# Kernel optimization log

Measured on AMD Instinct MI355X. Metric: run time of the kernel, lower is better.

The kernel has to match this reference:

```python
import jax, jax.numpy as jnp
import numpy as np

U, I, E, B, NNZ, N_LAYERS = 100000, 50000, 64, 3, 2400000, 3
N = U + I


def setup_inputs() -> dict:
    key = jax.random.key(0)
    ks = jax.random.split(key, 7)
    return {
        "user_emb": jax.random.normal(ks[0], (U, E), jnp.float32) * 0.1,
        "item_emb": jax.random.normal(ks[1], (I, E), jnp.float32) * 0.1,
        "W1": jax.random.normal(ks[2], (B, E, E // 4), jnp.float32) * 0.25,
        "W2": jax.random.normal(ks[3], (B, E // 4, 1), jnp.float32) * 0.5,
        "adj_vals": jax.random.uniform(ks[4], (B, NNZ), jnp.float32) * (1.0 / 16.0),
        "adj_rows": jax.random.randint(ks[5], (B, NNZ), 0, N, jnp.int32),
        "adj_cols": jax.random.randint(ks[6], (B, NNZ), 0, N, jnp.int32),
    }


def _spmm(vals, rows, cols, x):
    # sparse [N,N] @ dense [N,E] via gather + segment-sum over destination rows
    return jax.ops.segment_sum(vals[:, None] * x[cols], rows, num_segments=N)


def _propagate(vals, rows, cols, ego):
    acc = ego
    cur = ego
    for _ in range(N_LAYERS):
        cur = _spmm(vals, rows, cols, cur)
        acc = acc + cur
    return acc / float(N_LAYERS + 1)  # mean over stacked layer embeddings


def reference(user_emb, item_emb, W1, W2, adj_vals, adj_rows, adj_cols):
    ego = jnp.concatenate([user_emb, item_emb], axis=0)  # [N, E]
    # per-behavior LightGCN propagation (loop over small fixed B)
    beh = jnp.stack(
        [_propagate(adj_vals[i], adj_rows[i], adj_cols[i], ego) for i in range(B)],
        axis=1,
    )  # [N, B, E]

    def att_one(w1, w2):
        score = jnp.squeeze(jnp.tanh(beh @ w1) @ w2, -1)  # [N, B]
        a = jax.nn.softmax(score, axis=1)
        return jnp.einsum("nb,nbe->ne", a, beh)  # [N, E]

    bias = jax.vmap(att_one)(W1, W2)  # [B, N, E]
    user_beh_emb = bias[:, :U]  # [B, U, E]
    item_beh_emb = bias[:, U:]  # [B, I, E]
    return user_beh_emb, item_beh_emb
```

## Files before the change

kernel.cpp:

```cpp
#include <hip/hip_runtime.h>

#define UCNT 100000
#define ICNT 50000
#define BB   3
#define NNZE 2400000
#define NN   150000

#define P1B   16
#define PR1   9375
#define CAP1  156000
#define NBKT  (BB * P1B)
#define DEPTH 192
#define FCH   64
#define P1BLK 375
#define P1CH  6400
#define CSTR  16
#define HJ    8
#define P2J   128

#define SCAN_CHUNK 4096
#define CPB ((NN + SCAN_CHUNK - 1) / SCAN_CHUNK)

__global__ __launch_bounds__(256) void k_zero2(int* __restrict__ cnt,
                                               int* __restrict__ gcnt){
  long long i = (long long)blockIdx.x * blockDim.x + threadIdx.x;
  if (i < (long long)BB * NN) cnt[i] = 0;
  long long j = i - (long long)BB * NN;
  if (j >= 0 && j < NBKT * CSTR) gcnt[j] = 0;
}

__global__ __launch_bounds__(256) void k_cvt(const float* __restrict__ ue,
                                             const float* __restrict__ ie,
                                             unsigned* __restrict__ egob){
  long long w = (long long)blockIdx.x * blockDim.x + threadIdx.x;
  if (w >= (long long)NN * 32) return;
  long long n = w >> 5;
  int pr = (int)(w & 31);
  const float* src = (n < UCNT) ? (ue + n * 64) : (ie + (n - UCNT) * 64);
  float2 v = *(const float2*)(src + pr * 2);
  unsigned a = __float_as_uint(v.x); a += 0x7FFF + ((a >> 16) & 1);
  unsigned b = __float_as_uint(v.y); b += 0x7FFF + ((b >> 16) & 1);
  egob[w] = (a >> 16) | (b & 0xFFFF0000u);
}

__global__ __launch_bounds__(256) void k_p1(const int* __restrict__ rows,
                                            const int* __restrict__ cols,
                                            const float* __restrict__ vals,
                                            int* __restrict__ gcnt,
                                            int2* __restrict__ stg){
  __shared__ int2 lbuf[P1B][DEPTH];
  __shared__ int  lcnt[P1B];
  int tid = threadIdx.x, lane = tid & 63, wv = tid >> 6;
  int beh = blockIdx.x / P1BLK;
  int blk = blockIdx.x - beh * P1BLK;
  long long ebase = (long long)beh * NNZE + (long long)blk * P1CH;
  if (tid < P1B) lcnt[tid] = 0;
  __syncthreads();

  for (int r = 0; r < 13; ++r){
    int off = r * 512 + tid * 2;
    if (off < P1CH){
      long long i = ebase + off;
      int2  rr = *(const int2*)(rows + i);
      int2  cc = *(const int2*)(cols + i);
      float2 vv = *(const float2*)(vals + i);
      #pragma unroll
      for (int k = 0; k < 2; ++k){
        int row = k ? rr.y : rr.x;
        int col = k ? cc.y : cc.x;
        float val = k ? vv.y : vv.x;
        int part = row / PR1;
        int2 ent = make_int2(((row - part * PR1) << 18) | col,
                             __float_as_int(val));
        int p = atomicAdd(&lcnt[part], 1);
        if (p < DEPTH){
          lbuf[part][p] = ent;
        } else {
          int gb = atomicAdd(&gcnt[(beh * P1B + part) * CSTR], 1);
          if (gb < CAP1)
            stg[(long long)(beh * P1B + part) * CAP1 + gb] = ent;
        }
      }
    }
    __syncthreads();
    for (int pp = wv; pp < P1B; pp += 4){
      int n = min(lcnt[pp], DEPTH);
      int nf = n & ~(FCH - 1);
      if (nf > 0){
        int gb = 0;
        if (lane == 0) gb = atomicAdd(&gcnt[(beh * P1B + pp) * CSTR], nf);
        gb = __shfl(gb, 0);
        long long sb = (long long)(beh * P1B + pp) * CAP1;
        for (int k = lane; k < nf; k += 64)
          if (gb + k < CAP1) stg[sb + gb + k] = lbuf[pp][k];
        int res = n - nf;
        int2 t;
        if (lane < res) t = lbuf[pp][nf + lane];
        if (lane < res) lbuf[pp][lane] = t;
        if (lane == 0) lcnt[pp] = res;
      }
    }
    __syncthreads();
  }
  for (int pp = wv; pp < P1B; pp += 4){
    int n = min(lcnt[pp], DEPTH);
    if (n > 0){
      int gb = 0;
      if (lane == 0) gb = atomicAdd(&gcnt[(beh * P1B + pp) * CSTR], n);
      gb = __shfl(gb, 0);
      long long sb = (long long)(beh * P1B + pp) * CAP1;
      if (lane < n && gb + lane < CAP1) stg[sb + gb + lane] = lbuf[pp][lane];
    }
  }
}

__global__ __launch_bounds__(256) void k_hist3(const int* __restrict__ gcnt,
                                               const int2* __restrict__ stg,
                                               int* __restrict__ cnt){
  __shared__ int h[PR1];
  int bucket = blockIdx.x / HJ;
  int j = blockIdx.x - bucket * HJ;
  for (int i = threadIdx.x; i < PR1; i += 256) h[i] = 0;
  __syncthreads();
  int n = min(gcnt[bucket * CSTR], CAP1);
  const int2* st = stg + (long long)bucket * CAP1;
  int chunk = (n + HJ - 1) / HJ;
  int lo = j * chunk, hi = min(n, lo + chunk);
  for (int i = lo + threadIdx.x; i < hi; i += 256)
    atomicAdd(&h[(unsigned)st[i].x >> 18], 1);
  __syncthreads();
  int beh = bucket / P1B, part = bucket - beh * P1B;
  int* c = cnt + (long long)beh * NN + part * PR1;
  for (int i = threadIdx.x; i < PR1; i += 256){
    int v = h[i];
    if (v) atomicAdd(&c[i], v);
  }
}

__global__ __launch_bounds__(1024) void k_bsum(const int* __restrict__ cnt,
                                               int* __restrict__ bsum){
  int blk = blockIdx.x;
  int b = blk / CPB, ch = blk - b * CPB;
  const int* src = cnt + (long long)b * NN;
  int base = ch * SCAN_CHUNK + threadIdx.x * 4;
  int s = 0;
  #pragma unroll
  for (int k = 0; k < 4; ++k){
    int i = base + k;
    if (i < NN) s += src[i];
  }
  __shared__ int sd[1024];
  sd[threadIdx.x] = s;
  __syncthreads();
  for (int off = 512; off > 0; off >>= 1){
    if (threadIdx.x < off) sd[threadIdx.x] += sd[threadIdx.x + off];
    __syncthreads();
  }
  if (threadIdx.x == 0) bsum[blk] = sd[0];
}

__global__ __launch_bounds__(64) void k_bscan(const int* __restrict__ bsum,
                                              int* __restrict__ boff,
                                              int* __restrict__ rp){
  int b = threadIdx.x;
  if (b >= BB) return;
  int run = 0;
  for (int c = 0; c < CPB; ++c){
    boff[b * CPB + c] = run;
    run += bsum[b * CPB + c];
  }
  rp[(long long)b * (NN + 1) + NN] = run;
}

__global__ __launch_bounds__(1024) void k_scan2(const int* __restrict__ cnt,
                                                const int* __restrict__ boff,
                                                int* __restrict__ rp,
                                                int* __restrict__ tp){
  int blk = blockIdx.x;
  int b = blk / CPB, ch = blk - b * CPB;
  const int* src = cnt + (long long)b * NN;
  int* rpo = rp + (long long)b * (NN + 1);
  int* tpo = tp + (long long)b * NN;
  int base = ch * SCAN_CHUNK + threadIdx.x * 4;
  int v[4]; int tsum = 0;
  #pragma unroll
  for (int k = 0; k < 4; ++k){
    int i = base + k;
    v[k] = (i < NN) ? src[i] : 0;
    tsum += v[k];
  }
  __shared__ int sd[1024];
  sd[threadIdx.x] = tsum;
  __syncthreads();
  for (int off = 1; off < 1024; off <<= 1){
    int t = (threadIdx.x >= off) ? sd[threadIdx.x - off] : 0;
    __syncthreads();
    sd[threadIdx.x] += t;
    __syncthreads();
  }
  int excl = boff[blk] + sd[threadIdx.x] - tsum;
  #pragma unroll
  for (int k = 0; k < 4; ++k){
    int i = base + k;
    if (i < NN){ rpo[i] = excl; tpo[i] = excl; }
    excl += v[k];
  }
}

__global__ __launch_bounds__(256) void k_p2(const int* __restrict__ gcnt,
                                            const int2* __restrict__ stg,
                                            int* __restrict__ tp,
                                            int2* __restrict__ cpk,
                                            int L){
  int x = blockIdx.x & 7;
  int j = blockIdx.x >> 3;
  int bucket = L * 8 + x;
  int n = min(gcnt[bucket * CSTR], CAP1);
  int beh = bucket / P1B, part = bucket - beh * P1B;
  int rowbase = part * PR1;
  const int2* st = stg + (long long)bucket * CAP1;
  int* tpb = tp + (long long)beh * NN;
  int2* dst = cpk + (long long)beh * NNZE;
  int chunk = (n + P2J - 1) / P2J;
  int lo = j * chunk, hi = min(n, lo + chunk);
  for (int i = lo + threadIdx.x; i < hi; i += 256){
    int2 e = st[i];
    int row = rowbase + (int)((unsigned)e.x >> 18);
    int col = e.x & 0x3FFFF;
    int pos = atomicAdd(&tpb[row], 1);
    dst[pos] = make_int2(col, e.y);
  }
}

#define GB(NK)                                                              \
  {                                                                         \
    int   c[NK]; float v[NK]; float x[NK];                                  \
    _Pragma("unroll")                                                       \
    for (int k = 0; k < NK; ++k){                                           \
      int2 q = pk[e + k];                                                   \
      c[k] = __builtin_amdgcn_readfirstlane(q.x);                           \
      v[k] = __int_as_float(__builtin_amdgcn_readfirstlane(q.y));           \
    }                                                                       \
    _Pragma("unroll")                                                       \
    for (int k = 0; k < NK; ++k){                                           \
      unsigned w = xb[(long long)c[k] * 32 + (lane >> 1)];                  \
      x[k] = __uint_as_float((lane & 1) ? (w & 0xFFFF0000u) : (w << 16));   \
    }                                                                       \
    _Pragma("unroll")                                                       \
    for (int k = 0; k < NK; ++k){                                           \
      if (k & 1) sB = fmaf(v[k], x[k], sB);                                 \
      else       sA = fmaf(v[k], x[k], sA);                                 \
    }                                                                       \
    e += NK;                                                                \
  }

template<int MODE>
__global__ __launch_bounds__(256) void k_spmmB(const int* __restrict__ rp,
                                               const int2* __restrict__ cpk,
                                               const unsigned* __restrict__ xb,
                                               const float* __restrict__ ue,
                                               const float* __restrict__ ie,
                                               unsigned* __restrict__ dstb,
                                               float* __restrict__ acc,
                                               int b){
  int row = blockIdx.x * (blockDim.x >> 6) + (threadIdx.x >> 6);
  int lane = threadIdx.x & 63;
  row = __builtin_amdgcn_readfirstlane(row);
  const int* rpo = rp + (long long)b * (NN + 1);
  int s0 = __builtin_amdgcn_readfirstlane(rpo[row]);
  int s1 = __builtin_amdgcn_readfirstlane(rpo[row + 1]);
  const int2* pk = cpk + (long long)b * NNZE;
  float sA = 0.f, sB = 0.f;
  int e = s0;
  while (e + 16 <= s1) GB(16)
  if (e + 8 <= s1) GB(8)
  if (e + 4 <= s1) GB(4)
  if (e + 2 <= s1) GB(2)
  if (e < s1){
    int2 q = pk[e];
    int   c0 = __builtin_amdgcn_readfirstlane(q.x);
    float v0 = __int_as_float(__builtin_amdgcn_readfirstlane(q.y));
    unsigned w = xb[(long long)c0 * 32 + (lane >> 1)];
    float x0 = __uint_as_float((lane & 1) ? (w & 0xFFFF0000u) : (w << 16));
    sA = fmaf(v0, x0, sA);
  }
  float s = sA + sB;
  long long o = ((long long)b * NN + row) * 64 + lane;
  if (MODE == 0){
    float ego = (row < UCNT) ? ue[(long long)row * 64 + lane]
                             : ie[(long long)(row - UCNT) * 64 + lane];
    acc[o] = ego + s;
  } else {
    acc[o] += s;
  }
  if (MODE != 2){
    unsigned u = __float_as_uint(s);
    u += 0x7FFF + ((u >> 16) & 1);
    unsigned hb = u >> 16;
    unsigned ot = (unsigned)__shfl_xor((int)hb, 1);
    if (!(lane & 1))
      dstb[(long long)row * 32 + (lane >> 1)] = hb | (ot << 16);
  }
}

__device__ __forceinline__ float fast_tanh(float x){
  float xc = fminf(fmaxf(x, -15.f), 15.f);
  float t = __expf(2.f * xc);
  return (t - 1.f) / (t + 1.f);
}

__global__ __launch_bounds__(256) void k_score(const float* __restrict__ acc,
                                               const float* __restrict__ W1,
                                               const float* __restrict__ W2,
                                               float* __restrict__ scbuf){
  __shared__ float sW1[BB * 64 * 16];
  __shared__ float sW2[BB * 16];
  for (int i = threadIdx.x; i < BB * 64 * 16; i += blockDim.x) sW1[i] = W1[i];
  if (threadIdx.x < BB * 16) sW2[threadIdx.x] = W2[threadIdx.x];
  __syncthreads();
  int t = blockIdx.x * blockDim.x + threadIdx.x;
  if (t >= BB * NN) return;
  int b = t / NN;
  int n = t - b * NN;

  const float4* src = (const float4*)(acc + ((long long)b * NN + n) * 64);
  float4 v[16];
  #pragma unroll
  for (int c = 0; c < 16; ++c){
    v[c] = src[c];
    v[c].x *= 0.25f; v[c].y *= 0.25f; v[c].z *= 0.25f; v[c].w *= 0.25f;
  }
  for (int h = 0; h < BB; ++h){
    float hid[16];
    #pragma unroll
    for (int k = 0; k < 16; ++k) hid[k] = 0.f;
    #pragma unroll
    for (int c = 0; c < 16; ++c){
      const float* w = &sW1[h * 1024 + c * 64];
      #pragma unroll
      for (int k = 0; k < 16; ++k){
        hid[k] += v[c].x * w[k] + v[c].y * w[16 + k]
                + v[c].z * w[32 + k] + v[c].w * w[48 + k];
      }
    }
    float s = 0.f;
    #pragma unroll
    for (int k = 0; k < 16; ++k) s += fast_tanh(hid[k]) * sW2[h * 16 + k];
    scbuf[(long long)n * 9 + h * 3 + b] = s;
  }
}

__global__ __launch_bounds__(256) void k_att2(const float* __restrict__ acc,
                                              const float* __restrict__ scbuf,
                                              float* __restrict__ out){
  int t = blockIdx.x * blockDim.x + threadIdx.x;
  int n = t >> 4;
  int c = t & 15;
  if (n >= NN) return;
  float sc[9];
  #pragma unroll
  for (int i = 0; i < 9; ++i) sc[i] = scbuf[(long long)n * 9 + i];

  float a[BB][BB];
  #pragma unroll
  for (int h = 0; h < BB; ++h){
    float s0 = sc[h * 3], s1 = sc[h * 3 + 1], s2 = sc[h * 3 + 2];
    float m = fmaxf(fmaxf(s0, s1), s2);
    float e0 = __expf(s0 - m), e1 = __expf(s1 - m), e2 = __expf(s2 - m);
    float inv = 1.f / (e0 + e1 + e2);
    a[h][0] = e0 * inv; a[h][1] = e1 * inv; a[h][2] = e2 * inv;
  }
  float4 x0 = ((const float4*)(acc + ((long long)0 * NN + n) * 64))[c];
  float4 x1 = ((const float4*)(acc + ((long long)1 * NN + n) * 64))[c];
  float4 x2 = ((const float4*)(acc + ((long long)2 * NN + n) * 64))[c];
  x0.x *= 0.25f; x0.y *= 0.25f; x0.z *= 0.25f; x0.w *= 0.25f;
  x1.x *= 0.25f; x1.y *= 0.25f; x1.z *= 0.25f; x1.w *= 0.25f;
  x2.x *= 0.25f; x2.y *= 0.25f; x2.z *= 0.25f; x2.w *= 0.25f;
  #pragma unroll
  for (int h = 0; h < BB; ++h){
    float4 o;
    o.x = a[h][0]*x0.x + a[h][1]*x1.x + a[h][2]*x2.x;
    o.y = a[h][0]*x0.y + a[h][1]*x1.y + a[h][2]*x2.y;
    o.z = a[h][0]*x0.z + a[h][1]*x1.z + a[h][2]*x2.z;
    o.w = a[h][0]*x0.w + a[h][1]*x1.w + a[h][2]*x2.w;
    long long dst;
    if (n < UCNT) dst = ((long long)h * UCNT + n) * 64;
    else          dst = (long long)BB * UCNT * 64 + ((long long)h * ICNT + (n - UCNT)) * 64;
    ((float4*)(out + dst))[c] = o;
  }
}

extern "C" void kernel_launch(void* const* d_in, const int* in_sizes, int n_in,
                              void* d_out, int out_size, void* d_ws, size_t ws_size,
                              hipStream_t stream){
  const float* ue   = (const float*)d_in[0];
  const float* ie   = (const float*)d_in[1];
  const float* W1   = (const float*)d_in[2];
  const float* W2   = (const float*)d_in[3];
  const float* vals = (const float*)d_in[4];
  const int*   rows = (const int*)d_in[5];
  const int*   cols = (const int*)d_in[6];
  float* out = (float*)d_out;

  char* ws = (char*)d_ws;
  size_t off = 0;
  auto alloc = [&](size_t bytes){ void* p = ws + off; off += (bytes + 255) & ~(size_t)255; return p; };
  float*    acc   = (float*)alloc((size_t)BB * NN * 64 * 4);
  int2*     cpk   = (int2*)alloc((size_t)BB * NNZE * 8);
  int2*     stg   = (int2*)alloc((size_t)NBKT * CAP1 * 8);
  unsigned* egob  = (unsigned*)alloc((size_t)NN * 32 * 4);
  unsigned* layb0 = (unsigned*)alloc((size_t)NN * 32 * 4);
  unsigned* layb1 = (unsigned*)alloc((size_t)NN * 32 * 4);
  int*      rp    = (int*)alloc((size_t)BB * (NN + 1) * 4);
  int*      tp    = (int*)alloc((size_t)BB * NN * 4);
  int*      cnt   = (int*)alloc((size_t)BB * NN * 4);
  int*      bsum  = (int*)alloc((size_t)BB * CPB * 4);
  int*      boff  = (int*)alloc((size_t)BB * CPB * 4);
  int*      gcnt  = (int*)alloc((size_t)NBKT * CSTR * 4);
  float*    scbuf = (float*)alloc((size_t)NN * 9 * 4);
  (void)ws_size; (void)in_sizes; (void)n_in; (void)out_size;

  k_zero2<<<(BB * NN + NBKT * CSTR + 255) / 256, 256, 0, stream>>>(cnt, gcnt);
  k_cvt<<<(int)(((long long)NN * 32 + 255) / 256), 256, 0, stream>>>(ue, ie, egob);
  k_p1<<<BB * P1BLK, 256, 0, stream>>>(rows, cols, vals, gcnt, stg);
  k_hist3<<<NBKT * HJ, 256, 0, stream>>>(gcnt, stg, cnt);
  k_bsum<<<BB * CPB, 1024, 0, stream>>>(cnt, bsum);
  k_bscan<<<1, 64, 0, stream>>>(bsum, boff, rp);
  k_scan2<<<BB * CPB, 1024, 0, stream>>>(cnt, boff, rp, tp);
  for (int L = 0; L < 6; ++L)
    k_p2<<<8 * P2J, 256, 0, stream>>>(gcnt, stg, tp, cpk, L);

  for (int b = 0; b < BB; ++b){
    k_spmmB<0><<<NN / 4, 256, 0, stream>>>(rp, cpk, egob,  ue, ie, layb0, acc, b);
    k_spmmB<1><<<NN / 4, 256, 0, stream>>>(rp, cpk, layb0, ue, ie, layb1, acc, b);
    k_spmmB<2><<<NN / 4, 256, 0, stream>>>(rp, cpk, layb1, ue, ie, nullptr, acc, b);
  }
  k_score<<<(BB * NN + 255) / 256, 256, 0, stream>>>(acc, W1, W2, scbuf);
  k_att2<<<(NN * 16) / 256, 256, 0, stream>>>(acc, scbuf, out);
}
```

Measured before the change: 1.120 ms.

## Store per-layer bf16 outputs and drop fp32 accumulator read-modify-write in SpMM

The SpMM kernels no longer read the ego embedding or read-modify-write a large fp32 accumulator. Each layer now writes only its bf16 output into a 9-slot layer buffer. The score and attention kernels rebuild the layer mean by summing the bf16 ego and the three layer outputs. This cuts fp32 traffic in the propagation loop but adds more reads in the score and attention kernels. It also lowers accuracy, since the sum now uses the ego and the last layer in bf16 instead of fp32.

After: 1.054 ms. 1.06x faster.

```diff
diff --git a/kernel.cpp b/kernel.cpp
--- a/kernel.cpp
+++ b/kernel.cpp
@@ -20,6 +20,9 @@
 
 #define SCAN_CHUNK 4096
 #define CPB ((NN + SCAN_CHUNK - 1) / SCAN_CHUNK)
+
+__device__ __forceinline__ float blo(unsigned u){ return __uint_as_float(u << 16); }
+__device__ __forceinline__ float bhi(unsigned u){ return __uint_as_float(u & 0xFFFF0000u); }
 
 __global__ __launch_bounds__(256) void k_zero2(int* __restrict__ cnt,
                                                int* __restrict__ gcnt){
@@ -254,14 +257,10 @@
     e += NK;                                                                \
   }
 
-template<int MODE>
-__global__ __launch_bounds__(256) void k_spmmB(const int* __restrict__ rp,
+__global__ __launch_bounds__(256) void k_spmmL(const int* __restrict__ rp,
                                                const int2* __restrict__ cpk,
                                                const unsigned* __restrict__ xb,
-                                               const float* __restrict__ ue,
-                                               const float* __restrict__ ie,
                                                unsigned* __restrict__ dstb,
-                                               float* __restrict__ acc,
                                                int b){
   int row = blockIdx.x * (blockDim.x >> 6) + (threadIdx.x >> 6);
   int lane = threadIdx.x & 63;
@@ -285,22 +284,12 @@
     sA = fmaf(v0, x0, sA);
   }
   float s = sA + sB;
-  long long o = ((long long)b * NN + row) * 64 + lane;
-  if (MODE == 0){
-    float ego = (row < UCNT) ? ue[(long long)row * 64 + lane]
-                             : ie[(long long)(row - UCNT) * 64 + lane];
-    acc[o] = ego + s;
-  } else {
-    acc[o] += s;
-  }
-  if (MODE != 2){
-    unsigned u = __float_as_uint(s);
-    u += 0x7FFF + ((u >> 16) & 1);
-    unsigned hb = u >> 16;
-    unsigned ot = (unsigned)__shfl_xor((int)hb, 1);
-    if (!(lane & 1))
-      dstb[(long long)row * 32 + (lane >> 1)] = hb | (ot << 16);
-  }
+  unsigned u = __float_as_uint(s);
+  u += 0x7FFF + ((u >> 16) & 1);
+  unsigned hb = u >> 16;
+  unsigned ot = (unsigned)__shfl_xor((int)hb, 1);
+  if (!(lane & 1))
+    dstb[(long long)row * 32 + (lane >> 1)] = hb | (ot << 16);
 }
 
 __device__ __forceinline__ float fast_tanh(float x){
@@ -309,7 +298,13 @@
   return (t - 1.f) / (t + 1.f);
 }
 
-__global__ __launch_bounds__(256) void k_score(const float* __restrict__ acc,
+__device__ __forceinline__ void addbf(float4& a, float4& b, uint4 w){
+  a.x += blo(w.x); a.y += bhi(w.x); a.z += blo(w.y); a.w += bhi(w.y);
+  b.x += blo(w.z); b.y += bhi(w.z); b.z += blo(w.w); b.w += bhi(w.w);
+}
+
+__global__ __launch_bounds__(256) void k_score(const unsigned* __restrict__ egob,
+                                               const unsigned* __restrict__ layall,
                                                const float* __restrict__ W1,
                                                const float* __restrict__ W2,
                                                float* __restrict__ scbuf){
@@ -323,13 +318,28 @@
   int b = t / NN;
   int n = t - b * NN;
 
-  const float4* src = (const float4*)(acc + ((long long)b * NN + n) * 64);
+  const uint4* e4 = (const uint4*)(egob + (long long)n * 32);
+  const uint4* l0 = (const uint4*)(layall + ((long long)(b * 3 + 0) * NN + n) * 32);
+  const uint4* l1 = (const uint4*)(layall + ((long long)(b * 3 + 1) * NN + n) * 32);
+  const uint4* l2 = (const uint4*)(layall + ((long long)(b * 3 + 2) * NN + n) * 32);
   float4 v[16];
   #pragma unroll
+  for (int q = 0; q < 8; ++q){
+    uint4 w = e4[q];
+    v[2*q]   = make_float4(blo(w.x), bhi(w.x), blo(w.y), bhi(w.y));
+    v[2*q+1] = make_float4(blo(w.z), bhi(w.z), blo(w.w), bhi(w.w));
+  }
+  #pragma unroll
+  for (int q = 0; q < 8; ++q){ uint4 w = l0[q]; addbf(v[2*q], v[2*q+1], w); }
+  #pragma unroll
+  for (int q = 0; q < 8; ++q){ uint4 w = l1[q]; addbf(v[2*q], v[2*q+1], w); }
+  #pragma unroll
+  for (int q = 0; q < 8; ++q){ uint4 w = l2[q]; addbf(v[2*q], v[2*q+1], w); }
+  #pragma unroll
   for (int c = 0; c < 16; ++c){
-    v[c] = src[c];
     v[c].x *= 0.25f; v[c].y *= 0.25f; v[c].z *= 0.25f; v[c].w *= 0.25f;
   }
+
   for (int h = 0; h < BB; ++h){
     float hid[16];
     #pragma unroll
@@ -350,7 +360,8 @@
   }
 }
 
-__global__ __launch_bounds__(256) void k_att2(const float* __restrict__ acc,
+__global__ __launch_bounds__(256) void k_att2(const unsigned* __restrict__ egob,
+                                              const unsigned* __restrict__ layall,
                                               const float* __restrict__ scbuf,
                                               float* __restrict__ out){
   int t = blockIdx.x * blockDim.x + threadIdx.x;
@@ -370,19 +381,29 @@
     float inv = 1.f / (e0 + e1 + e2);
     a[h][0] = e0 * inv; a[h][1] = e1 * inv; a[h][2] = e2 * inv;
   }
-  float4 x0 = ((const float4*)(acc + ((long long)0 * NN + n) * 64))[c];
-  float4 x1 = ((const float4*)(acc + ((long long)1 * NN + n) * 64))[c];
-  float4 x2 = ((const float4*)(acc + ((long long)2 * NN + n) * 64))[c];
-  x0.x *= 0.25f; x0.y *= 0.25f; x0.z *= 0.25f; x0.w *= 0.25f;
-  x1.x *= 0.25f; x1.y *= 0.25f; x1.z *= 0.25f; x1.w *= 0.25f;
-  x2.x *= 0.25f; x2.y *= 0.25f; x2.z *= 0.25f; x2.w *= 0.25f;
+  long long ro = (long long)n * 32 + c * 2;
+  unsigned eg0 = egob[ro], eg1 = egob[ro + 1];
+  float4 x[BB];
+  #pragma unroll
+  for (int bb = 0; bb < BB; ++bb){
+    const unsigned* p0 = layall + ((long long)(bb * 3 + 0) * NN) * 32 + ro;
+    const unsigned* p1 = layall + ((long long)(bb * 3 + 1) * NN) * 32 + ro;
+    const unsigned* p2 = layall + ((long long)(bb * 3 + 2) * NN) * 32 + ro;
+    unsigned u00 = p0[0], u01 = p0[1];
+    unsigned u10 = p1[0], u11 = p1[1];
+    unsigned u20 = p2[0], u21 = p2[1];
+    x[bb].x = 0.25f * (blo(eg0) + blo(u00) + blo(u10) + blo(u20));
+    x[bb].y = 0.25f * (bhi(eg0) + bhi(u00) + bhi(u10) + bhi(u20));
+    x[bb].z = 0.25f * (blo(eg1) + blo(u01) + blo(u11) + blo(u21));
+    x[bb].w = 0.25f * (bhi(eg1) + bhi(u01) + bhi(u11) + bhi(u21));
+  }
   #pragma unroll
   for (int h = 0; h < BB; ++h){
     float4 o;
-    o.x = a[h][0]*x0.x + a[h][1]*x1.x + a[h][2]*x2.x;
-    o.y = a[h][0]*x0.y + a[h][1]*x1.y + a[h][2]*x2.y;
-    o.z = a[h][0]*x0.z + a[h][1]*x1.z + a[h][2]*x2.z;
-    o.w = a[h][0]*x0.w + a[h][1]*x1.w + a[h][2]*x2.w;
+    o.x = a[h][0]*x[0].x + a[h][1]*x[1].x + a[h][2]*x[2].x;
+    o.y = a[h][0]*x[0].y + a[h][1]*x[1].y + a[h][2]*x[2].y;
+    o.z = a[h][0]*x[0].z + a[h][1]*x[1].z + a[h][2]*x[2].z;
+    o.w = a[h][0]*x[0].w + a[h][1]*x[1].w + a[h][2]*x[2].w;
     long long dst;
     if (n < UCNT) dst = ((long long)h * UCNT + n) * 64;
     else          dst = (long long)BB * UCNT * 64 + ((long long)h * ICNT + (n - UCNT)) * 64;
@@ -405,19 +426,17 @@
   char* ws = (char*)d_ws;
   size_t off = 0;
   auto alloc = [&](size_t bytes){ void* p = ws + off; off += (bytes + 255) & ~(size_t)255; return p; };
-  float*    acc   = (float*)alloc((size_t)BB * NN * 64 * 4);
-  int2*     cpk   = (int2*)alloc((size_t)BB * NNZE * 8);
-  int2*     stg   = (int2*)alloc((size_t)NBKT * CAP1 * 8);
-  unsigned* egob  = (unsigned*)alloc((size_t)NN * 32 * 4);
-  unsigned* layb0 = (unsigned*)alloc((size_t)NN * 32 * 4);
-  unsigned* layb1 = (unsigned*)alloc((size_t)NN * 32 * 4);
-  int*      rp    = (int*)alloc((size_t)BB * (NN + 1) * 4);
-  int*      tp    = (int*)alloc((size_t)BB * NN * 4);
-  int*      cnt   = (int*)alloc((size_t)BB * NN * 4);
-  int*      bsum  = (int*)alloc((size_t)BB * CPB * 4);
-  int*      boff  = (int*)alloc((size_t)BB * CPB * 4);
-  int*      gcnt  = (int*)alloc((size_t)NBKT * CSTR * 4);
-  float*    scbuf = (float*)alloc((size_t)NN * 9 * 4);
+  int2*     cpk    = (int2*)alloc((size_t)BB * NNZE * 8);
+  int2*     stg    = (int2*)alloc((size_t)NBKT * CAP1 * 8);
+  unsigned* egob   = (unsigned*)alloc((size_t)NN * 32 * 4);
+  unsigned* layall = (unsigned*)alloc((size_t)9 * NN * 32 * 4);
+  int*      rp     = (int*)alloc((size_t)BB * (NN + 1) * 4);
+  int*      tp     = (int*)alloc((size_t)BB * NN * 4);
+  int*      cnt    = (int*)alloc((size_t)BB * NN * 4);
+  int*      bsum   = (int*)alloc((size_t)BB * CPB * 4);
+  int*      boff   = (int*)alloc((size_t)BB * CPB * 4);
+  int*      gcnt   = (int*)alloc((size_t)NBKT * CSTR * 4);
+  float*    scbuf  = (float*)alloc((size_t)NN * 9 * 4);
   (void)ws_size; (void)in_sizes; (void)n_in; (void)out_size;
 
   k_zero2<<<(BB * NN + NBKT * CSTR + 255) / 256, 256, 0, stream>>>(cnt, gcnt);
@@ -430,11 +449,13 @@
   for (int L = 0; L < 6; ++L)
     k_p2<<<8 * P2J, 256, 0, stream>>>(gcnt, stg, tp, cpk, L);
 
-  for (int b = 0; b < BB; ++b){
-    k_spmmB<0><<<NN / 4, 256, 0, stream>>>(rp, cpk, egob,  ue, ie, layb0, acc, b);
-    k_spmmB<1><<<NN / 4, 256, 0, stream>>>(rp, cpk, layb0, ue, ie, layb1, acc, b);
-    k_spmmB<2><<<NN / 4, 256, 0, stream>>>(rp, cpk, layb1, ue, ie, nullptr, acc, b);
-  }
-  k_score<<<(BB * NN + 255) / 256, 256, 0, stream>>>(acc, W1, W2, scbuf);
-  k_att2<<<(NN * 16) / 256, 256, 0, stream>>>(acc, scbuf, out);
-}
+  for (int l = 0; l < 3; ++l)
+    for (int b = 0; b < BB; ++b){
+      const unsigned* src = (l == 0) ? egob
+                          : (layall + (size_t)(b * 3 + l - 1) * NN * 32);
+      unsigned* dst = layall + (size_t)(b * 3 + l) * NN * 32;
+      k_spmmL<<<NN / 4, 256, 0, stream>>>(rp, cpk, src, dst, b);
+    }
+  k_score<<<(BB * NN + 255) / 256, 256, 0, stream>>>(egob, layall, W1, W2, scbuf);
+  k_att2<<<(NN * 16) / 256, 256, 0, stream>>>(egob, layall, scbuf, out);
+}
```
